# Kernel tuning notes

Hardware: AMD Instinct MI355X
Metric: run time of the kernel (lower is better)

The kernel has to match this reference:

```python
import jax, jax.numpy as jnp
import numpy as np

N_E = 1024
E_DIM = 256
BETA = 0.25
BATCH = 131072


def setup_inputs() -> dict:
    key = jax.random.key(0)
    k1, k2 = jax.random.split(key)
    z = jax.random.normal(k1, (BATCH, E_DIM), dtype=jnp.float32)
    # matches nn.Embedding init uniform_(-1/n_e, 1/n_e)
    emb_weight = jax.random.uniform(k2, (N_E, E_DIM), dtype=jnp.float32,
                                    minval=-1.0 / N_E, maxval=1.0 / N_E)
    return {"z": z, "emb_weight": emb_weight}


def reference(z, emb_weight):
    # z: [B, e_dim] (the module's unsqueeze/permute/view is an identity reshape)
    # squared L2 distances: [B, n_e]
    d = (jnp.sum(z * z, axis=1, keepdims=True)
         + jnp.sum(emb_weight * emb_weight, axis=1)
         - 2.0 * jnp.matmul(z, emb_weight.T))
    min_encoding_indices = jnp.argmin(d, axis=1)            # [B]
    min_encodings = jax.nn.one_hot(min_encoding_indices, N_E, dtype=z.dtype)  # [B, n_e]
    z_q = jnp.matmul(min_encodings, emb_weight)             # [B, e_dim]

    sg = jax.lax.stop_gradient
    loss = jnp.mean((sg(z_q) - z) ** 2) + BETA * jnp.mean((z_q - sg(z)) ** 2)

    # straight-through estimator
    z_q_ste = z + sg(z_q - z)

    e_mean = jnp.mean(min_encodings, axis=0)                # [n_e]
    perplexity = jnp.exp(-jnp.sum(e_mean * jnp.log(e_mean + 1e-10)))

    return (z_q_ste, loss, min_encoding_indices[:, None], perplexity)
```

## Files before the change

### kernel.cpp

```cpp
#include <hip/hip_runtime.h>

typedef __attribute__((ext_vector_type(8))) __bf16 bf16x8;
typedef __attribute__((ext_vector_type(4))) float f32x4;
typedef __attribute__((ext_vector_type(8))) unsigned short u16x8;

#define B_ROWS 131072
#define EDIM   256
#define N_E    1024
#define BMR    64
#define CHUNKS 32
#define CAP    16
#define OROWS  32

#define OUT1 ((size_t)B_ROWS * EDIM)
#define OUT2 (OUT1 + 1)
#define OUT3 (OUT2 + B_ROWS)

#define WS_EMBT  0
#define WS_ESQ   524288
#define WS_COUNT 528384
#define WS_LOSS  532480

__device__ __forceinline__ unsigned short f2bf(float f) {
    unsigned u = __float_as_uint(f);
    return (unsigned short)((u + 0x7FFFu + ((u >> 16) & 1u)) >> 16);
}
__device__ __forceinline__ unsigned encf(float f) {
    unsigned u = __float_as_uint(f);
    return u ^ (unsigned)(((int)u >> 31) | 0x80000000);
}
__device__ __forceinline__ float decf(unsigned x) {
    return (x & 0x80000000u) ? __uint_as_float(x ^ 0x80000000u)
                             : __uint_as_float(~x);
}
__device__ __forceinline__ float med3f(float a, float b, float c) {
#if __has_builtin(__builtin_amdgcn_fmed3f)
    return __builtin_amdgcn_fmed3f(a, b, c);
#else
    return fmaxf(fminf(a, b), fminf(fmaxf(a, b), c));
#endif
}

__device__ inline float pw128_sq(const float* p) {
    float4 v0 = *(const float4*)p, v1 = *(const float4*)(p + 4);
    float r[8];
    r[0] = __fmul_rn(v0.x, v0.x); r[1] = __fmul_rn(v0.y, v0.y);
    r[2] = __fmul_rn(v0.z, v0.z); r[3] = __fmul_rn(v0.w, v0.w);
    r[4] = __fmul_rn(v1.x, v1.x); r[5] = __fmul_rn(v1.y, v1.y);
    r[6] = __fmul_rn(v1.z, v1.z); r[7] = __fmul_rn(v1.w, v1.w);
    for (int i = 8; i < 128; i += 8) {
        v0 = *(const float4*)(p + i); v1 = *(const float4*)(p + i + 4);
        r[0] = __fadd_rn(r[0], __fmul_rn(v0.x, v0.x));
        r[1] = __fadd_rn(r[1], __fmul_rn(v0.y, v0.y));
        r[2] = __fadd_rn(r[2], __fmul_rn(v0.z, v0.z));
        r[3] = __fadd_rn(r[3], __fmul_rn(v0.w, v0.w));
        r[4] = __fadd_rn(r[4], __fmul_rn(v1.x, v1.x));
        r[5] = __fadd_rn(r[5], __fmul_rn(v1.y, v1.y));
        r[6] = __fadd_rn(r[6], __fmul_rn(v1.z, v1.z));
        r[7] = __fadd_rn(r[7], __fmul_rn(v1.w, v1.w));
    }
    float s01 = __fadd_rn(r[0], r[1]), s23 = __fadd_rn(r[2], r[3]);
    float s45 = __fadd_rn(r[4], r[5]), s67 = __fadd_rn(r[6], r[7]);
    return __fadd_rn(__fadd_rn(s01, s23), __fadd_rn(s45, s67));
}

__device__ inline float exact_d(const float* zp, const float* ep, float zsq, float eq) {
    const float4* z4 = (const float4*)zp;
    const float4* e4 = (const float4*)ep;
    float acc = 0.f;
#pragma unroll 8
    for (int k = 0; k < 64; ++k) {
        float4 a = z4[k], b = e4[k];
        acc = __fmaf_rn(a.x, b.x, acc);
        acc = __fmaf_rn(a.y, b.y, acc);
        acc = __fmaf_rn(a.z, b.z, acc);
        acc = __fmaf_rn(a.w, b.w, acc);
    }
    return __fsub_rn(__fadd_rn(zsq, eq), 2.0f * acc);
}

__global__ void prep_emb(const float* __restrict__ emb,
                         unsigned short* __restrict__ embT,
                         float* __restrict__ esqg)
{
    int n = blockIdx.x, t = threadIdx.x;
    const float4 v = ((const float4*)(emb + (size_t)n * EDIM))[t];
    ushort4 o = { f2bf(v.x), f2bf(v.y), f2bf(v.z), f2bf(v.w) };
    int g = t >> 1, j0 = (t & 1) * 4;
    *(ushort4*)(embT + ((size_t)g * N_E + n) * 8 + j0) = o;
    if (t < 2) {
        float h = pw128_sq(emb + (size_t)n * EDIM + 128 * t);
        float ho = __shfl_xor(h, 1);
        if (t == 0) esqg[n] = __fadd_rn(h, ho);
    }
}

#define INS(s_, code_, r_)                                                  \
    {                                                                       \
        bool lt1 = (s_) < bd1[r_];                                          \
        bool lt2 = (s_) < bd2[r_];                                          \
        bd3[r_] = med3f((s_), bd2[r_], bd3[r_]);                            \
        bd2[r_] = med3f((s_), bd1[r_], bd2[r_]);                            \
        bd1[r_] = fminf((s_), bd1[r_]);                                     \
        int low_ = cp_[r_] & 0xFFFF;                                        \
        cp_[r_] = lt1 ? ((code_) | (low_ << 16))                            \
                      : (lt2 ? (low_ | ((code_) << 16)) : cp_[r_]);         \
    }

__global__ __launch_bounds__(256, 4) void vq_search(
    const float* __restrict__ z, const float* __restrict__ emb,
    const unsigned short* __restrict__ embT, const float* __restrict__ esqg,
    float* __restrict__ out, unsigned int* __restrict__ count)
{
    __shared__ float esq_s[N_E];
    __shared__ float zsq_s[BMR], S_s[BMR];
    __shared__ unsigned cnt[BMR];
    __shared__ unsigned short list[BMR][CAP];
    __shared__ int rowbest[BMR];
    __shared__ unsigned long long fb4[4];

    const int tid  = threadIdx.x;
    const int blk  = blockIdx.x;
    const int lane = tid & 63;
    const int w    = tid >> 6;
    const int col  = lane & 15;
    const int quad = lane >> 4;
    const int row0 = w * 16;

    const float* zb = z + (size_t)blk * BMR * EDIM;

    for (int i = tid; i < N_E; i += 256) esq_s[i] = esqg[i];
    if (tid < BMR) cnt[tid] = 0u;

    bf16x8 afr[8];
    {
        int row = row0 + col;
#pragma unroll
        for (int ks = 0; ks < 8; ++ks) {
            const float* p = zb + row * EDIM + ((ks * 4 + quad) << 3);
            float4 a0 = *(const float4*)p;
            float4 a1 = *(const float4*)(p + 4);
            u16x8 t = { f2bf(a0.x), f2bf(a0.y), f2bf(a0.z), f2bf(a0.w),
                        f2bf(a1.x), f2bf(a1.y), f2bf(a1.z), f2bf(a1.w) };
            afr[ks] = *(bf16x8*)&t;
        }
    }

    if (tid < 128) {
        int row = tid >> 1, half = tid & 1;
        const float* p = zb + row * EDIM + half * 128;
        float h = pw128_sq(p);
        const float4* p4 = (const float4*)p;
        float4 sv = {0.f, 0.f, 0.f, 0.f};
#pragma unroll
        for (int jj = 0; jj < 32; ++jj) {
            float4 vv = p4[jj];
            sv.x += fabsf(vv.x); sv.y += fabsf(vv.y);
            sv.z += fabsf(vv.z); sv.w += fabsf(vv.w);
        }
        float sa = (sv.x + sv.y) + (sv.z + sv.w);
        float ho = __shfl_xor(h, 1);
        float so = __shfl_xor(sa, 1);
        if (half == 0) {
            zsq_s[row] = __fadd_rn(h, ho);
            S_s[row]   = (sa + so) * 1.001f;
        }
    }
    __syncthreads();

    int koff[8];
#pragma unroll
    for (int ks = 0; ks < 8; ++ks)
        koff[ks] = ((((ks * 4 + quad) << 10) + col) << 3);

    float bd1[4], bd2[4], bd3[4];
    int   cp_[4];
#pragma unroll
    for (int r = 0; r < 4; ++r) {
        bd1[r] = INFINITY; bd2[r] = INFINITY; bd3[r] = INFINITY; cp_[r] = 0;
    }

    for (int c = 0; c < CHUNKS; ++c) {
        const unsigned short* cb = embT + (c << 8);
        {
            u16x8 bfr[8];
#pragma unroll
            for (int ks = 0; ks < 8; ++ks)
                bfr[ks] = *(const u16x8*)(cb + koff[ks]);
            f32x4 acc = {0.f, 0.f, 0.f, 0.f};
#pragma unroll
            for (int ks = 0; ks < 8; ++ks)
                acc = __builtin_amdgcn_mfma_f32_16x16x32_bf16(afr[ks], *(bf16x8*)&bfr[ks], acc, 0, 0, 0);
            const int codeN = (c << 5) + col;
            const float eqv = esq_s[codeN];
#pragma unroll
            for (int r = 0; r < 4; ++r) {
                float s = __fmaf_rn(-2.0f, acc[r], eqv);
                INS(s, codeN, r);
            }
        }
        {
            u16x8 bfr[8];
#pragma unroll
            for (int ks = 0; ks < 8; ++ks)
                bfr[ks] = *(const u16x8*)(cb + koff[ks] + 128);
            f32x4 acc = {0.f, 0.f, 0.f, 0.f};
#pragma unroll
            for (int ks = 0; ks < 8; ++ks)
                acc = __builtin_amdgcn_mfma_f32_16x16x32_bf16(afr[ks], *(bf16x8*)&bfr[ks], acc, 0, 0, 0);
            const int codeN = (c << 5) + 16 + col;
            const float eqv = esq_s[codeN];
#pragma unroll
            for (int r = 0; r < 4; ++r) {
                float s = __fmaf_rn(-2.0f, acc[r], eqv);
                INS(s, codeN, r);
            }
        }
    }

    float th[4];
#pragma unroll
    for (int r = 0; r < 4; ++r) {
        unsigned long long kk =
            ((unsigned long long)encf(bd1[r]) << 32) | (unsigned)(cp_[r] & 0xFFFF);
#pragma unroll
        for (int msk = 1; msk <= 8; msk <<= 1) {
            unsigned long long o = __shfl_xor(kk, msk);
            if (o < kk) kk = o;
        }
        int row = row0 + quad * 4 + r;
        th[r] = decf((unsigned)(kk >> 32)) + (S_s[row] * (1.0f / 131072.0f) + 1e-4f);
    }

#pragma unroll
    for (int r = 0; r < 4; ++r) {
        int row = row0 + quad * 4 + r;
        if (__builtin_expect(bd1[r] <= th[r], 0)) {
            unsigned i = atomicAdd(&cnt[row], 1u);
            if (i < CAP) list[row][i] = (unsigned short)(cp_[r] & 0xFFFF);
        }
        if (__builtin_expect(bd2[r] <= th[r], 0)) {
            unsigned i = atomicAdd(&cnt[row], 1u);
            if (i < CAP) list[row][i] = (unsigned short)((unsigned)cp_[r] >> 16);
        }
        if (__builtin_expect(bd3[r] <= th[r], 0))
            atomicAdd(&cnt[row], 1000u);
    }
    __syncthreads();

    {
        int row = tid >> 2, j = tid & 3;
        int cn = (int)cnt[row];
        unsigned long long bkey = ~0ull;
        float zq = zsq_s[row];
        const float* zrow = zb + row * EDIM;
        if (cn <= CAP) {
            for (int i = j; i < cn; i += 4) {
                int n = (int)list[row][i];
                float d = exact_d(zrow, emb + (size_t)n * EDIM, zq, esq_s[n]);
                unsigned long long k2 = ((unsigned long long)encf(d) << 32) | (unsigned)n;
                if (k2 < bkey) bkey = k2;
            }
        }
#pragma unroll
        for (int m = 1; m <= 2; m <<= 1) {
            unsigned long long o = __shfl_xor(bkey, m);
            if (o < bkey) bkey = o;
        }
        if (j == 0) rowbest[row] = (cn <= CAP) ? (int)(bkey & 0xFFFFFFFFu) : -1;
    }
    __syncthreads();

    for (int r = 0; r < BMR; ++r) {
        if (rowbest[r] != -1) continue;
        const float* zr = zb + r * EDIM;
        float zqr = zsq_s[r];
        unsigned long long k = ~0ull;
        for (int ci = 0; ci < 4; ++ci) {
            int n = tid + ci * 256;
            float d = exact_d(zr, emb + (size_t)n * EDIM, zqr, esq_s[n]);
            unsigned long long k2 = ((unsigned long long)encf(d) << 32) | (unsigned)n;
            if (k2 < k) k = k2;
        }
#pragma unroll
        for (int msk = 1; msk <= 32; msk <<= 1) {
            unsigned long long o = __shfl_xor(k, msk);
            if (o < k) k = o;
        }
        if (lane == 0) fb4[w] = k;
        __syncthreads();
        if (tid == 0) {
            unsigned long long m0 = fb4[0] < fb4[1] ? fb4[0] : fb4[1];
            unsigned long long m1 = fb4[2] < fb4[3] ? fb4[2] : fb4[3];
            rowbest[r] = (int)((m0 < m1 ? m0 : m1) & 0xFFFFFFFFu);
        }
        __syncthreads();
    }

    if (tid < BMR) {
        int bn = rowbest[tid];
        out[OUT2 + (size_t)blk * BMR + tid] = (float)bn;
        atomicAdd(&count[bn], 1u);
    }
}

__global__ void vq_output(const float* __restrict__ z, const float* __restrict__ emb,
                          float* __restrict__ out, double* __restrict__ lossSum)
{
    __shared__ double red4s[4];
    const int tid = threadIdx.x;
    const int blk = blockIdx.x;
    const int lane = tid & 63;
    const int w   = tid >> 6;
    const int row = tid >> 3;
    const int q   = tid & 7;
    const size_t grow = (size_t)blk * OROWS + row;
    const int bn = (int)out[OUT2 + grow];
    const float4* zp4 = (const float4*)(z + grow * EDIM);
    const float4* ebr = (const float4*)(emb + (size_t)bn * EDIM);
    float4* outr = (float4*)(out + grow * EDIM);
    double lacc = 0.0;
#pragma unroll
    for (int i = 0; i < 8; ++i) {
        int k4 = q + i * 8;
        float4 zv = zp4[k4];
        float4 ev = ebr[k4];
        float4 o; float sd;
        sd = __fsub_rn(ev.x, zv.x); o.x = __fadd_rn(zv.x, sd); lacc += (double)__fmul_rn(sd, sd);
        sd = __fsub_rn(ev.y, zv.y); o.y = __fadd_rn(zv.y, sd); lacc += (double)__fmul_rn(sd, sd);
        sd = __fsub_rn(ev.z, zv.z); o.z = __fadd_rn(zv.z, sd); lacc += (double)__fmul_rn(sd, sd);
        sd = __fsub_rn(ev.w, zv.w); o.w = __fadd_rn(zv.w, sd); lacc += (double)__fmul_rn(sd, sd);
        outr[k4] = o;
    }
#pragma unroll
    for (int msk = 1; msk <= 32; msk <<= 1) lacc += __shfl_xor(lacc, msk);
    if (lane == 0) red4s[w] = lacc;
    __syncthreads();
    if (tid == 0) atomicAdd(lossSum, red4s[0] + red4s[1] + red4s[2] + red4s[3]);
}

__global__ void vq_finalize(const unsigned int* __restrict__ count,
                            const double* __restrict__ lossSum,
                            float* __restrict__ out)
{
    __shared__ double red[1024];
    int t = threadIdx.x;
    double em = (double)count[t] * (1.0 / 131072.0);
    red[t] = em * log(em + 1e-10);
    __syncthreads();
    for (int s = 512; s > 0; s >>= 1) {
        if (t < s) red[t] += red[t + s];
        __syncthreads();
    }
    if (t == 0) {
        out[OUT3] = (float)exp(-red[0]);
        double m = lossSum[0] * (1.0 / 33554432.0);
        out[OUT1] = (float)(1.25 * m);
    }
}

extern "C" void kernel_launch(void* const* d_in, const int* in_sizes, int n_in,
                              void* d_out, int out_size, void* d_ws, size_t ws_size,
                              hipStream_t stream) {
    const float* z   = (const float*)d_in[0];
    const float* emb = (const float*)d_in[1];
    float* out = (float*)d_out;

    unsigned short* embT = (unsigned short*)((char*)d_ws + WS_EMBT);
    float* esqg          = (float*)((char*)d_ws + WS_ESQ);
    unsigned int* count  = (unsigned int*)((char*)d_ws + WS_COUNT);
    double* lossSum      = (double*)((char*)d_ws + WS_LOSS);

    hipMemsetAsync((char*)d_ws + WS_COUNT, 0, 4104, stream);
    prep_emb<<<N_E, 64, 0, stream>>>(emb, embT, esqg);
    vq_search<<<B_ROWS / BMR, 256, 0, stream>>>(z, emb, embT, esqg, out, count);
    vq_output<<<B_ROWS / OROWS, 256, 0, stream>>>(z, emb, out, lossSum);
    vq_finalize<<<1, 1024, 0, stream>>>(count, lossSum, out);
}
```

Measured before the change: 392.2 us.

## Split search kernel into bf16 scan and exact rescore kernels via scratch records

The fused search kernel is split in two. The first kernel runs the bf16 MFMA scan and writes each row's candidate count and list as a packed record into the output buffer, which serves as scratch. The second kernel recomputes the row squared norms and rescores the candidates exactly in fp32. This lightens the scan kernel's shared memory and code, which may help occupancy, at the cost of an extra launch, a round trip through global memory for the records, and a second read of z.

Result: no change. 391.1 us (-0.3%).

```diff
diff --git a/kernel.cpp b/kernel.cpp
--- a/kernel.cpp
+++ b/kernel.cpp
@@ -15,6 +15,7 @@
 #define OUT1 ((size_t)B_ROWS * EDIM)
 #define OUT2 (OUT1 + 1)
 #define OUT3 (OUT2 + B_ROWS)
+#define SCR_WORDS 10
 
 #define WS_EMBT  0
 #define WS_ESQ   524288
@@ -107,17 +108,14 @@
                       : (lt2 ? (low_ | ((code_) << 16)) : cp_[r_]);         \
     }
 
-__global__ __launch_bounds__(256, 4) void vq_search(
-    const float* __restrict__ z, const float* __restrict__ emb,
-    const unsigned short* __restrict__ embT, const float* __restrict__ esqg,
-    float* __restrict__ out, unsigned int* __restrict__ count)
+__global__ __launch_bounds__(256, 4) void vq_scan(
+    const float* __restrict__ z, const unsigned short* __restrict__ embT,
+    const float* __restrict__ esqg, float* __restrict__ out)
 {
     __shared__ float esq_s[N_E];
-    __shared__ float zsq_s[BMR], S_s[BMR];
+    __shared__ float S_s[BMR];
     __shared__ unsigned cnt[BMR];
     __shared__ unsigned short list[BMR][CAP];
-    __shared__ int rowbest[BMR];
-    __shared__ unsigned long long fb4[4];
 
     const int tid  = threadIdx.x;
     const int blk  = blockIdx.x;
@@ -148,9 +146,7 @@
 
     if (tid < 128) {
         int row = tid >> 1, half = tid & 1;
-        const float* p = zb + row * EDIM + half * 128;
-        float h = pw128_sq(p);
-        const float4* p4 = (const float4*)p;
+        const float4* p4 = (const float4*)(zb + row * EDIM + half * 128);
         float4 sv = {0.f, 0.f, 0.f, 0.f};
 #pragma unroll
         for (int jj = 0; jj < 32; ++jj) {
@@ -159,12 +155,8 @@
             sv.z += fabsf(vv.z); sv.w += fabsf(vv.w);
         }
         float sa = (sv.x + sv.y) + (sv.z + sv.w);
-        float ho = __shfl_xor(h, 1);
         float so = __shfl_xor(sa, 1);
-        if (half == 0) {
-            zsq_s[row] = __fadd_rn(h, ho);
-            S_s[row]   = (sa + so) * 1.001f;
-        }
+        if (half == 0) S_s[row] = (sa + so) * 1.001f;
     }
     __syncthreads();
 
@@ -248,15 +240,51 @@
     }
     __syncthreads();
 
+    if (tid < BMR) {
+        unsigned* rec = (unsigned*)out + ((size_t)blk * BMR + tid) * SCR_WORDS;
+        rec[0] = cnt[tid];
+#pragma unroll
+        for (int k = 0; k < 8; ++k)
+            rec[1 + k] = (unsigned)list[tid][2 * k] | ((unsigned)list[tid][2 * k + 1] << 16);
+    }
+}
+
+__global__ void vq_rescore(
+    const float* __restrict__ z, const float* __restrict__ emb,
+    const float* __restrict__ esqg, float* __restrict__ out,
+    unsigned int* __restrict__ count)
+{
+    __shared__ float esq_s[N_E];
+    __shared__ float zsq_s[BMR];
+    __shared__ int rowbest[BMR];
+    __shared__ unsigned long long fb4[4];
+
+    const int tid  = threadIdx.x;
+    const int blk  = blockIdx.x;
+    const int lane = tid & 63;
+    const int w    = tid >> 6;
+    const float* zb = z + (size_t)blk * BMR * EDIM;
+
+    for (int i = tid; i < N_E; i += 256) esq_s[i] = esqg[i];
+    __syncthreads();
+
     {
         int row = tid >> 2, j = tid & 3;
-        int cn = (int)cnt[row];
+        const float* zrow = zb + row * EDIM;
+        float h = (j < 2) ? pw128_sq(zrow + 128 * j) : 0.f;
+        int base = lane & ~3;
+        float v0 = __shfl(h, base);
+        float v1 = __shfl(h, base + 1);
+        float zq = __fadd_rn(v0, v1);
+        if (j == 0) zsq_s[row] = zq;
+
+        const unsigned* rec = (const unsigned*)out + ((size_t)blk * BMR + row) * SCR_WORDS;
+        int cn = (int)rec[0];
         unsigned long long bkey = ~0ull;
-        float zq = zsq_s[row];
-        const float* zrow = zb + row * EDIM;
         if (cn <= CAP) {
             for (int i = j; i < cn; i += 4) {
-                int n = (int)list[row][i];
+                unsigned pr = rec[1 + (i >> 1)];
+                int n = (int)((i & 1) ? (pr >> 16) : (pr & 0xFFFF));
                 float d = exact_d(zrow, emb + (size_t)n * EDIM, zq, esq_s[n]);
                 unsigned long long k2 = ((unsigned long long)encf(d) << 32) | (unsigned)n;
                 if (k2 < bkey) bkey = k2;
@@ -373,7 +401,8 @@
 
     hipMemsetAsync((char*)d_ws + WS_COUNT, 0, 4104, stream);
     prep_emb<<<N_E, 64, 0, stream>>>(emb, embT, esqg);
-    vq_search<<<B_ROWS / BMR, 256, 0, stream>>>(z, emb, embT, esqg, out, count);
+    vq_scan<<<B_ROWS / BMR, 256, 0, stream>>>(z, embT, esqg, out);
+    vq_rescore<<<B_ROWS / BMR, 256, 0, stream>>>(z, emb, esqg, out, count);
     vq_output<<<B_ROWS / OROWS, 256, 0, stream>>>(z, emb, out, lossSum);
     vq_finalize<<<1, 1024, 0, stream>>>(count, lossSum, out);
 }
```

## Fuse output/loss kernel into search kernel and defer row norms

Applied to the files above, without the earlier changes.

Merges the separate output kernel (STE output, loss accumulation) into the search kernel, so each block writes z_q and accumulates loss for its own 64 rows right after choosing indices. This avoids a second pass over z and the reload of indices from global memory. The squared row norm is now computed only for rows that need exact refinement, and rows with a single candidate skip the distance computation entirely. The trade-off is more work per block, which may raise register pressure or tail time in the search kernel.

After: 368.5 us. 1.06x faster.

```diff
diff --git a/kernel.cpp b/kernel.cpp
--- a/kernel.cpp
+++ b/kernel.cpp
@@ -10,7 +10,6 @@
 #define BMR    64
 #define CHUNKS 32
 #define CAP    16
-#define OROWS  32
 
 #define OUT1 ((size_t)B_ROWS * EDIM)
 #define OUT2 (OUT1 + 1)
@@ -107,17 +106,20 @@
                       : (lt2 ? (low_ | ((code_) << 16)) : cp_[r_]);         \
     }
 
-__global__ __launch_bounds__(256, 4) void vq_search(
+__global__ __launch_bounds__(256, 4) void vq_main(
     const float* __restrict__ z, const float* __restrict__ emb,
     const unsigned short* __restrict__ embT, const float* __restrict__ esqg,
-    float* __restrict__ out, unsigned int* __restrict__ count)
+    float* __restrict__ out, unsigned int* __restrict__ count,
+    double* __restrict__ lossSum)
 {
     __shared__ float esq_s[N_E];
-    __shared__ float zsq_s[BMR], S_s[BMR];
+    __shared__ float S_s[BMR];
     __shared__ unsigned cnt[BMR];
     __shared__ unsigned short list[BMR][CAP];
     __shared__ int rowbest[BMR];
+    __shared__ float zq_fb;
     __shared__ unsigned long long fb4[4];
+    __shared__ double red4s[4];
 
     const int tid  = threadIdx.x;
     const int blk  = blockIdx.x;
@@ -148,9 +150,7 @@
 
     if (tid < 128) {
         int row = tid >> 1, half = tid & 1;
-        const float* p = zb + row * EDIM + half * 128;
-        float h = pw128_sq(p);
-        const float4* p4 = (const float4*)p;
+        const float4* p4 = (const float4*)(zb + row * EDIM + half * 128);
         float4 sv = {0.f, 0.f, 0.f, 0.f};
 #pragma unroll
         for (int jj = 0; jj < 32; ++jj) {
@@ -159,12 +159,8 @@
             sv.z += fabsf(vv.z); sv.w += fabsf(vv.w);
         }
         float sa = (sv.x + sv.y) + (sv.z + sv.w);
-        float ho = __shfl_xor(h, 1);
         float so = __shfl_xor(sa, 1);
-        if (half == 0) {
-            zsq_s[row] = __fadd_rn(h, ho);
-            S_s[row]   = (sa + so) * 1.001f;
-        }
+        if (half == 0) S_s[row] = (sa + so) * 1.001f;
     }
     __syncthreads();
 
@@ -251,30 +247,41 @@
     {
         int row = tid >> 2, j = tid & 3;
         int cn = (int)cnt[row];
-        unsigned long long bkey = ~0ull;
-        float zq = zsq_s[row];
-        const float* zrow = zb + row * EDIM;
-        if (cn <= CAP) {
+        if (cn > CAP) {
+            if (j == 0) rowbest[row] = -1;
+        } else if (cn == 1) {
+            if (j == 0) rowbest[row] = (int)list[row][0];
+        } else {
+            const float* zrow = zb + row * EDIM;
+            float h = (j < 2) ? pw128_sq(zrow + 128 * j) : 0.f;
+            int base = lane & ~3;
+            float v0 = __shfl(h, base);
+            float v1 = __shfl(h, base + 1);
+            float zq = __fadd_rn(v0, v1);
+            unsigned long long bkey = ~0ull;
             for (int i = j; i < cn; i += 4) {
                 int n = (int)list[row][i];
                 float d = exact_d(zrow, emb + (size_t)n * EDIM, zq, esq_s[n]);
                 unsigned long long k2 = ((unsigned long long)encf(d) << 32) | (unsigned)n;
                 if (k2 < bkey) bkey = k2;
             }
-        }
-#pragma unroll
-        for (int m = 1; m <= 2; m <<= 1) {
-            unsigned long long o = __shfl_xor(bkey, m);
-            if (o < bkey) bkey = o;
-        }
-        if (j == 0) rowbest[row] = (cn <= CAP) ? (int)(bkey & 0xFFFFFFFFu) : -1;
+#pragma unroll
+            for (int m = 1; m <= 2; m <<= 1) {
+                unsigned long long o = __shfl_xor(bkey, m);
+                if (o < bkey) bkey = o;
+            }
+            if (j == 0) rowbest[row] = (int)(bkey & 0xFFFFFFFFu);
+        }
     }
     __syncthreads();
 
     for (int r = 0; r < BMR; ++r) {
         if (rowbest[r] != -1) continue;
         const float* zr = zb + r * EDIM;
-        float zqr = zsq_s[r];
+        if (tid == 0)
+            zq_fb = __fadd_rn(pw128_sq(zr), pw128_sq(zr + 128));
+        __syncthreads();
+        float zqr = zq_fb;
         unsigned long long k = ~0ull;
         for (int ci = 0; ci < 4; ++ci) {
             int n = tid + ci * 256;
@@ -289,54 +296,43 @@
         }
         if (lane == 0) fb4[w] = k;
         __syncthreads();
-        if (tid == 0) {
-            unsigned long long m0 = fb4[0] < fb4[1] ? fb4[0] : fb4[1];
-            unsigned long long m1 = fb4[2] < fb4[3] ? fb4[2] : fb4[3];
-            rowbest[r] = (int)((m0 < m1 ? m0 : m1) & 0xFFFFFFFFu);
-        }
-        __syncthreads();
-    }
-
-    if (tid < BMR) {
-        int bn = rowbest[tid];
-        out[OUT2 + (size_t)blk * BMR + tid] = (float)bn;
-        atomicAdd(&count[bn], 1u);
-    }
-}
-
-__global__ void vq_output(const float* __restrict__ z, const float* __restrict__ emb,
-                          float* __restrict__ out, double* __restrict__ lossSum)
-{
-    __shared__ double red4s[4];
-    const int tid = threadIdx.x;
-    const int blk = blockIdx.x;
-    const int lane = tid & 63;
-    const int w   = tid >> 6;
-    const int row = tid >> 3;
-    const int q   = tid & 7;
-    const size_t grow = (size_t)blk * OROWS + row;
-    const int bn = (int)out[OUT2 + grow];
-    const float4* zp4 = (const float4*)(z + grow * EDIM);
-    const float4* ebr = (const float4*)(emb + (size_t)bn * EDIM);
-    float4* outr = (float4*)(out + grow * EDIM);
-    double lacc = 0.0;
-#pragma unroll
-    for (int i = 0; i < 8; ++i) {
-        int k4 = q + i * 8;
-        float4 zv = zp4[k4];
-        float4 ev = ebr[k4];
-        float4 o; float sd;
-        sd = __fsub_rn(ev.x, zv.x); o.x = __fadd_rn(zv.x, sd); lacc += (double)__fmul_rn(sd, sd);
-        sd = __fsub_rn(ev.y, zv.y); o.y = __fadd_rn(zv.y, sd); lacc += (double)__fmul_rn(sd, sd);
-        sd = __fsub_rn(ev.z, zv.z); o.z = __fadd_rn(zv.z, sd); lacc += (double)__fmul_rn(sd, sd);
-        sd = __fsub_rn(ev.w, zv.w); o.w = __fadd_rn(zv.w, sd); lacc += (double)__fmul_rn(sd, sd);
-        outr[k4] = o;
-    }
-#pragma unroll
-    for (int msk = 1; msk <= 32; msk <<= 1) lacc += __shfl_xor(lacc, msk);
-    if (lane == 0) red4s[w] = lacc;
-    __syncthreads();
-    if (tid == 0) atomicAdd(lossSum, red4s[0] + red4s[1] + red4s[2] + red4s[3]);
+        if (tid == 0) rowbest[r] = (int)((fb4[0] < fb4[1] ? fb4[0] : fb4[1]) <
+                                         (fb4[2] < fb4[3] ? fb4[2] : fb4[3])
+                                         ? (fb4[0] < fb4[1] ? fb4[0] : fb4[1])
+                                         : (fb4[2] < fb4[3] ? fb4[2] : fb4[3]));
+        __syncthreads();
+    }
+
+    {
+        const int row = tid >> 2, q = tid & 3;
+        const size_t grow = (size_t)blk * BMR + row;
+        const int bn = rowbest[row];
+        const float4* zp4 = (const float4*)(zb + row * EDIM);
+        const float4* ebr = (const float4*)(emb + (size_t)bn * EDIM);
+        float4* outr = (float4*)(out + grow * EDIM);
+        double lacc = 0.0;
+#pragma unroll
+        for (int i = 0; i < 16; ++i) {
+            int k4 = q + i * 4;
+            float4 zv = zp4[k4];
+            float4 ev = ebr[k4];
+            float4 o; float sd;
+            sd = __fsub_rn(ev.x, zv.x); o.x = __fadd_rn(zv.x, sd); lacc += (double)__fmul_rn(sd, sd);
+            sd = __fsub_rn(ev.y, zv.y); o.y = __fadd_rn(zv.y, sd); lacc += (double)__fmul_rn(sd, sd);
+            sd = __fsub_rn(ev.z, zv.z); o.z = __fadd_rn(zv.z, sd); lacc += (double)__fmul_rn(sd, sd);
+            sd = __fsub_rn(ev.w, zv.w); o.w = __fadd_rn(zv.w, sd); lacc += (double)__fmul_rn(sd, sd);
+            outr[k4] = o;
+        }
+        if (q == 0) {
+            out[OUT2 + grow] = (float)bn;
+            atomicAdd(&count[bn], 1u);
+        }
+#pragma unroll
+        for (int msk = 1; msk <= 32; msk <<= 1) lacc += __shfl_xor(lacc, msk);
+        if (lane == 0) red4s[w] = lacc;
+        __syncthreads();
+        if (tid == 0) atomicAdd(lossSum, red4s[0] + red4s[1] + red4s[2] + red4s[3]);
+    }
 }
 
 __global__ void vq_finalize(const unsigned int* __restrict__ count,
@@ -373,7 +369,6 @@
 
     hipMemsetAsync((char*)d_ws + WS_COUNT, 0, 4104, stream);
     prep_emb<<<N_E, 64, 0, stream>>>(emb, embT, esqg);
-    vq_search<<<B_ROWS / BMR, 256, 0, stream>>>(z, emb, embT, esqg, out, count);
-    vq_output<<<B_ROWS / OROWS, 256, 0, stream>>>(z, emb, out, lossSum);
+    vq_main<<<B_ROWS / BMR, 256, 0, stream>>>(z, emb, embT, esqg, out, count, lossSum);
     vq_finalize<<<1, 1024, 0, stream>>>(count, lossSum, out);
 }
```
